# Kernel tuning notes

Measured on AMD Instinct MI355X. Metric: run time of the kernel, lower is better.

Reference implementation:

```python
import jax, jax.numpy as jnp
import numpy as np
import math

D_MODEL = 1024
NUM_HEADS = 16
HEAD_DIM = D_MODEL // NUM_HEADS
WINDOW = 5  # positions j with i - W//2 <= j <= i + W//2 are visible


def setup_inputs() -> dict:
    key = jax.random.key(0)
    ks = jax.random.split(key, 9)
    B, S = 2, 2048
    x = jax.random.normal(ks[0], (B, S, D_MODEL), dtype=jnp.float32)
    # Xavier-uniform linear weights [out, in] (torch convention), zero biases
    lim = math.sqrt(6.0 / (D_MODEL + D_MODEL))
    def w(k):
        return jax.random.uniform(k, (D_MODEL, D_MODEL), dtype=jnp.float32, minval=-lim, maxval=lim)
    return {
        'x': x,
        'Wq': w(ks[1]), 'bq': jnp.zeros((D_MODEL,), jnp.float32),
        'Wk': w(ks[2]), 'bk': jnp.zeros((D_MODEL,), jnp.float32),
        'Wv': w(ks[3]), 'bv': jnp.zeros((D_MODEL,), jnp.float32),
        'Wo': w(ks[4]), 'bo': jnp.zeros((D_MODEL,), jnp.float32),
    }


def reference(x, Wq, bq, Wk, bk, Wv, bv, Wo, bo):
    B, S, D = x.shape
    H, hd = NUM_HEADS, HEAD_DIM
    half = WINDOW // 2

    def proj(W, b):
        # torch Linear: y = x @ W.T + b ; split heads -> [B, H, S, hd]
        return (jnp.einsum('bsd,ed->bse', x, W) + b).reshape(B, S, H, hd).transpose(0, 2, 1, 3)

    q = proj(Wq, bq)
    k = proj(Wk, bk)
    v = proj(Wv, bv)

    scores = jnp.einsum('bhqd,bhkd->bhqk', q, k) / jnp.sqrt(jnp.asarray(hd, x.dtype))
    i = jnp.arange(S)[:, None]
    j = jnp.arange(S)[None, :]
    band = (j >= i - half) & (j <= i + half)  # [S, S] local window mask
    scores = jnp.where(band, scores, jnp.asarray(-1e9, x.dtype))
    attn = jax.nn.softmax(scores, axis=-1)  # dropout is identity in eval mode
    out = jnp.einsum('bhqk,bhkd->bhqd', attn, v)
    out = out.transpose(0, 2, 1, 3).reshape(B, S, D)
    return jnp.einsum('bsd,ed->bse', out, Wo) + bo
```

## Files before the change

### kernel.cpp

```cpp
#include <hip/hip_runtime.h>
#include <hip/hip_bf16.h>

typedef __bf16 bf16_t;
typedef __bf16 bf16x4 __attribute__((ext_vector_type(4)));
typedef __bf16 bf16x8 __attribute__((ext_vector_type(8)));
typedef float f32x4 __attribute__((ext_vector_type(4)));

#define S_LEN 2048
#define DMODEL 1024
#define NHEADS 16
#define HDIM 64
#define BROWS 4096
#define QKVN 3072

__device__ __forceinline__ void async16(const void* g, void* l) {
  __builtin_amdgcn_global_load_lds(
      (const __attribute__((address_space(1))) void*)g,
      (__attribute__((address_space(3))) void*)l, 16, 0, 0);
}

__global__ __launch_bounds__(256) void cvt_all_kernel(
    const float* __restrict__ x, const float* __restrict__ Wq,
    const float* __restrict__ Wk, const float* __restrict__ Wv,
    const float* __restrict__ Wo, bf16_t* __restrict__ dst) {
  const int i = blockIdx.x * 256 + threadIdx.x;
  constexpr int XN4 = (BROWS * DMODEL) / 4;
  constexpr int WN4 = (DMODEL * DMODEL) / 4;
  const float* src;
  size_t off;
  if (i < XN4) {
    src = x;
    off = (size_t)i;
  } else {
    const int wi = i - XN4;
    const int w = wi >> 18;
    off = (size_t)(wi & (WN4 - 1));
    src = (w == 0) ? Wq : (w == 1) ? Wk : (w == 2) ? Wv : Wo;
  }
  const float4 v = *(const float4*)(src + off * 4);
  bf16x4 o;
  o[0] = (bf16_t)v.x;
  o[1] = (bf16_t)v.y;
  o[2] = (bf16_t)v.z;
  o[3] = (bf16_t)v.w;
  *(bf16x4*)(dst + (size_t)i * 4) = o;
}

#define BARR __builtin_amdgcn_s_barrier()
#define SB0 __builtin_amdgcn_sched_barrier(0)
#define VMC3 asm volatile("s_waitcnt vmcnt(3)" ::: "memory")
#define VMC0 asm volatile("s_waitcnt vmcnt(0)" ::: "memory")

__global__ __launch_bounds__(512, 2) void gemm_qkv256_kernel(
    const bf16_t* __restrict__ A, const bf16_t* __restrict__ W,
    const float* __restrict__ bq, const float* __restrict__ bk,
    const float* __restrict__ bv, bf16_t* __restrict__ C) {
  constexpr int Kd = 1024;
  __shared__ char lds[114688];
  char* ldsA = lds;
  char* ldsB = lds + 65536;

  const int m0 = blockIdx.x * 256;
  const int n0 = blockIdx.y * 192;

  const int tid = threadIdx.x;
  const int lane = tid & 63;
  const int wid = tid >> 6;
  const int wr = wid >> 2;
  const int wc = wid & 3;
  const int fr = lane & 15;
  const int l16 = lane >> 4;

  f32x4 acc[8][3] = {};
  bf16x8 aS0[4][2], aS1[4][2], bB[3][2];

  auto stageA = [&](int buf, int h, int kt) {
#pragma unroll
    for (int l = 0; l < 2; ++l) {
      const int idx = l * 512 + tid;
      const int r = idx >> 3;
      const int slot = idx & 7;
      async16((const char*)(A + (size_t)(m0 + h * 128 + r) * Kd + kt * 64 +
                            ((slot ^ (r & 7)) << 3)),
              ldsA + buf * 32768 + h * 16384 + r * 128 + slot * 16);
    }
  };
  auto stageB = [&](int buf, int th, int kt) {
    const int r = tid >> 3;
    const int slot = tid & 7;
    async16((const char*)(W + (size_t)(n0 + th * 64 + r) * Kd + kt * 64 +
                          ((slot ^ (r & 7)) << 3)),
            ldsB + buf * 24576 + th * 8192 + r * 128 + slot * 16);
  };

  auto rdA = [&](int buf, int row, int ks) -> bf16x8 {
    return *(const bf16x8*)(ldsA + buf * 32768 + row * 128 +
                            ((((ks << 2) + l16) ^ (row & 7)) << 4));
  };
  auto rdB = [&](int buf, int row, int ks) -> bf16x8 {
    return *(const bf16x8*)(ldsB + buf * 24576 + row * 128 +
                            ((((ks << 2) + l16) ^ (row & 7)) << 4));
  };

#define RDA_TO(AS, MH, BUF)                                              \
  _Pragma("unroll") for (int m_ = 0; m_ < 4; ++m_)                       \
      _Pragma("unroll") for (int ks_ = 0; ks_ < 2; ++ks_) AS[m_][ks_] =  \
          rdA(BUF, wr * 128 + (MH)*64 + m_ * 16 + fr, ks_);
#define RDB(NF0, NC, BUF)                                                \
  _Pragma("unroll") for (int n_ = 0; n_ < (NC); ++n_)                    \
      _Pragma("unroll") for (int ks_ = 0; ks_ < 2; ++ks_)                \
          bB[(NF0) + n_][ks_] =                                          \
              rdB(BUF, wc * 48 + ((NF0) + n_) * 16 + fr, ks_);
#define MMAQ(AS, MH, NF0, NC)                                                 \
  _Pragma("unroll") for (int m_ = 0; m_ < 4; ++m_)                            \
      _Pragma("unroll") for (int n_ = 0; n_ < (NC); ++n_) {                   \
    acc[(MH)*4 + m_][(NF0) + n_] = __builtin_amdgcn_mfma_f32_16x16x32_bf16(   \
        AS[m_][0], bB[(NF0) + n_][0], acc[(MH)*4 + m_][(NF0) + n_], 0, 0, 0); \
    acc[(MH)*4 + m_][(NF0) + n_] = __builtin_amdgcn_mfma_f32_16x16x32_bf16(   \
        AS[m_][1], bB[(NF0) + n_][1], acc[(MH)*4 + m_][(NF0) + n_], 0, 0, 0); \
  }

  stageA(0, 0, 0);
  stageA(0, 1, 0);
  stageB(0, 0, 0);
  stageB(0, 1, 0);
  stageB(0, 2, 0);
  stageB(1, 0, 1);
  stageB(1, 1, 1);
  stageB(1, 2, 1);
  VMC3;
  BARR;

#pragma unroll 1
  for (int i = 0; i < 8; ++i) {
    const int t0 = 2 * i, t1 = 2 * i + 1;
    const bool st = (i < 7);
    RDA_TO(aS0, 0, 0);
    RDB(0, 2, 0);
    RDA_TO(aS1, 1, 0);
    stageA(1, 0, t1);
    SB0;
    BARR;
    __builtin_amdgcn_s_setprio(1);
    MMAQ(aS0, 0, 0, 2);
    __builtin_amdgcn_s_setprio(0);
    BARR;
    RDB(2, 1, 0);
    stageA(1, 1, t1);
    SB0;
    BARR;
    __builtin_amdgcn_s_setprio(1);
    MMAQ(aS0, 0, 2, 1);
    __builtin_amdgcn_s_setprio(0);
    BARR;
    if (st) stageB(0, 0, t0 + 2);
    SB0;
    BARR;
    __builtin_amdgcn_s_setprio(1);
    MMAQ(aS1, 1, 0, 2);
    __builtin_amdgcn_s_setprio(0);
    BARR;
    if (st) {
      stageB(0, 1, t0 + 2);
      stageB(0, 2, t0 + 2);
    }
    SB0;
    __builtin_amdgcn_s_setprio(1);
    MMAQ(aS1, 1, 2, 1);
    __builtin_amdgcn_s_setprio(0);
    SB0;
    if (st) {
      VMC3;
    } else {
      VMC0;
    }
    BARR;
    RDA_TO(aS0, 0, 1);
    RDB(0, 2, 1);
    RDA_TO(aS1, 1, 1);
    if (st) stageA(0, 0, t0 + 2);
    SB0;
    BARR;
    __builtin_amdgcn_s_setprio(1);
    MMAQ(aS0, 0, 0, 2);
    __builtin_amdgcn_s_setprio(0);
    BARR;
    RDB(2, 1, 1);
    if (st) stageA(0, 1, t0 + 2);
    SB0;
    BARR;
    __builtin_amdgcn_s_setprio(1);
    MMAQ(aS0, 0, 2, 1);
    __builtin_amdgcn_s_setprio(0);
    BARR;
    if (st) stageB(1, 0, t1 + 2);
    SB0;
    BARR;
    __builtin_amdgcn_s_setprio(1);
    MMAQ(aS1, 1, 0, 2);
    __builtin_amdgcn_s_setprio(0);
    BARR;
    if (st) {
      stageB(1, 1, t1 + 2);
      stageB(1, 2, t1 + 2);
    }
    SB0;
    __builtin_amdgcn_s_setprio(1);
    MMAQ(aS1, 1, 2, 1);
    __builtin_amdgcn_s_setprio(0);
    SB0;
    if (st) VMC3;
    BARR;
  }
#undef RDA_TO
#undef RDB
#undef MMAQ

  const int cr = l16 * 4;
#pragma unroll
  for (int nf = 0; nf < 3; ++nf) {
    const int col = n0 + wc * 48 + nf * 16 + fr;
    const int mat = col >> 10;
    const float* bp = (mat == 0) ? bq : (mat == 1) ? bk : bv;
    const float bval = bp[col & 1023];
#pragma unroll
    for (int mf = 0; mf < 8; ++mf) {
      const int row = m0 + wr * 128 + mf * 16 + cr;
#pragma unroll
      for (int r = 0; r < 4; ++r)
        C[(size_t)(row + r) * QKVN + col] = (bf16_t)(acc[mf][nf][r] + bval);
    }
  }
}

__global__ __launch_bounds__(512) void gemm_o_kernel(
    const bf16_t* __restrict__ Adat, const bf16_t* __restrict__ W,
    const float* __restrict__ bias, float* __restrict__ out) {
  constexpr int Kd = 1024, Nd = 1024, BK = 32, NT = Kd / BK;
  __shared__ bf16_t ldsA[2][128 * BK];
  __shared__ bf16_t ldsB[2][128 * BK];

  const int m0 = blockIdx.x * 128;
  const int n0 = blockIdx.y * 128;

  const int tid = threadIdx.x;
  const int lane = tid & 63;
  const int wid = tid >> 6;
  const int wr = wid >> 2;
  const int wc = wid & 3;
  const int fr = lane & 15;
  const int ko = (lane >> 4) * 8;

  f32x4 acc[4][2] = {};

  auto stage = [&](int buf, int t) {
    const int k0 = t * BK;
    const int row = tid >> 2;
    const int kb = (tid & 3) * 16;
    async16((const char*)(Adat + (size_t)(m0 + row) * Kd + k0) + kb,
            (char*)ldsA[buf] + row * 64 + kb);
    async16((const char*)(W + (size_t)(n0 + row) * Kd + k0) + kb,
            (char*)ldsB[buf] + row * 64 + kb);
  };

  auto compute = [&](int buf) {
    bf16x8 af[4], bf[2];
#pragma unroll
    for (int i = 0; i < 4; ++i)
      af[i] = *(const bf16x8*)(ldsA[buf] + (wr * 64 + i * 16 + fr) * BK + ko);
#pragma unroll
    for (int j = 0; j < 2; ++j)
      bf[j] = *(const bf16x8*)(ldsB[buf] + (wc * 32 + j * 16 + fr) * BK + ko);
#pragma unroll
    for (int i = 0; i < 4; ++i)
#pragma unroll
      for (int j = 0; j < 2; ++j)
        acc[i][j] = __builtin_amdgcn_mfma_f32_16x16x32_bf16(af[i], bf[j],
                                                            acc[i][j], 0, 0, 0);
  };

  stage(0, 0);
  __syncthreads();
#pragma unroll 1
  for (int t = 0; t < NT; ++t) {
    if (t + 1 < NT) stage((t + 1) & 1, t + 1);
    compute(t & 1);
    __syncthreads();
  }

  const int cr = (lane >> 4) * 4;
#pragma unroll
  for (int j = 0; j < 2; ++j) {
    const int col = n0 + wc * 32 + j * 16 + fr;
    const float bval = bias[col];
#pragma unroll
    for (int i = 0; i < 4; ++i) {
#pragma unroll
      for (int r = 0; r < 4; ++r) {
        const int row = m0 + wr * 64 + i * 16 + cr + r;
        out[(size_t)row * Nd + col] = acc[i][j][r] + bval;
      }
    }
  }
}

#define CHUNK 256
#define TROWS 260

__global__ __launch_bounds__(256) void attn_kernel(
    const bf16_t* __restrict__ QKV, bf16_t* __restrict__ ctx) {
  __shared__ bf16_t ldsK[TROWS * HDIM];
  __shared__ bf16_t ldsV[TROWS * HDIM];

  const int tid = threadIdx.x;
  const int blk = blockIdx.x;
  const int chunk = blk & 7;
  const int bh = blk >> 3;
  const int h = bh & (NHEADS - 1);
  const int b = bh >> 4;
  const int s0 = chunk * CHUNK;

  const bf16_t* Kb = QKV + (size_t)b * S_LEN * QKVN + DMODEL + h * HDIM;
  const bf16_t* Vb = QKV + (size_t)b * S_LEN * QKVN + 2 * DMODEL + h * HDIM;

#pragma unroll
  for (int j = 0; j < 9; ++j) {
    const int i = j * 256 + tid;
    if (i < TROWS * 8) {
      const int tr = i >> 3;
      const int slot = i & 7;
      const int c = slot ^ (tr & 7);
      int gs = s0 - 2 + tr;
      gs = (gs < 0) ? 0 : (gs >= S_LEN ? S_LEN - 1 : gs);
      async16((const char*)(Kb + (size_t)gs * QKVN) + c * 16,
              (char*)ldsK + i * 16);
      async16((const char*)(Vb + (size_t)gs * QKVN) + c * 16,
              (char*)ldsV + i * 16);
    }
  }

  const int s = s0 + tid;
  const bf16_t* Qrow = QKV + ((size_t)(b * S_LEN) + s) * QKVN + h * HDIM;
  bf16x8 q8[8];
#pragma unroll
  for (int c = 0; c < 8; ++c) q8[c] = *(const bf16x8*)(Qrow + c * 8);
  float qf[64];
#pragma unroll
  for (int c = 0; c < 8; ++c)
#pragma unroll
    for (int e = 0; e < 8; ++e) qf[c * 8 + e] = (float)q8[c][e];

  __syncthreads();

  float sc[5];
#pragma unroll
  for (int jj = 0; jj < 5; ++jj) {
    const int tr = tid + jj;
    float d = 0.f;
#pragma unroll
    for (int c = 0; c < 8; ++c) {
      const bf16x8 k8 = *(const bf16x8*)(ldsK + tr * HDIM + (c ^ (tr & 7)) * 8);
#pragma unroll
      for (int e = 0; e < 8; ++e) d += qf[c * 8 + e] * (float)k8[e];
    }
    const int j = s - 2 + jj;
    sc[jj] = (j < 0 || j >= S_LEN) ? -1e30f : d * 0.125f;
  }

  float m = sc[0];
#pragma unroll
  for (int jj = 1; jj < 5; ++jj) m = fmaxf(m, sc[jj]);
  float p[5], l = 0.f;
#pragma unroll
  for (int jj = 0; jj < 5; ++jj) {
    p[jj] = __expf(sc[jj] - m);
    l += p[jj];
  }
  const float inv = 1.0f / l;
#pragma unroll
  for (int jj = 0; jj < 5; ++jj) p[jj] *= inv;

  float o[64];
#pragma unroll
  for (int e = 0; e < 64; ++e) o[e] = 0.f;
#pragma unroll
  for (int jj = 0; jj < 5; ++jj) {
    const int tr = tid + jj;
    const float pj = p[jj];
#pragma unroll
    for (int c = 0; c < 8; ++c) {
      const bf16x8 v8 = *(const bf16x8*)(ldsV + tr * HDIM + (c ^ (tr & 7)) * 8);
#pragma unroll
      for (int e = 0; e < 8; ++e) o[c * 8 + e] += pj * (float)v8[e];
    }
  }

  bf16_t* Crow = (bf16_t*)ctx + ((size_t)(b * S_LEN) + s) * DMODEL + h * HDIM;
#pragma unroll
  for (int c = 0; c < 8; ++c) {
    bf16x8 ov;
#pragma unroll
    for (int e = 0; e < 8; ++e) ov[e] = (bf16_t)o[c * 8 + e];
    *(bf16x8*)(Crow + c * 8) = ov;
  }
}

extern "C" void kernel_launch(void* const* d_in, const int* in_sizes, int n_in,
                              void* d_out, int out_size, void* d_ws,
                              size_t ws_size, hipStream_t stream) {
  const float* x = (const float*)d_in[0];
  const float* Wq = (const float*)d_in[1];
  const float* bq = (const float*)d_in[2];
  const float* Wk = (const float*)d_in[3];
  const float* bk = (const float*)d_in[4];
  const float* Wv = (const float*)d_in[5];
  const float* bv = (const float*)d_in[6];
  const float* Wo = (const float*)d_in[7];
  const float* bo = (const float*)d_in[8];
  float* out = (float*)d_out;

  const size_t mat = (size_t)BROWS * DMODEL;
  const size_t wmat = (size_t)DMODEL * DMODEL;
  bf16_t* xb = (bf16_t*)d_ws;
  bf16_t* Wqkv = xb + mat;
  bf16_t* Wob = Wqkv + 3 * wmat;
  bf16_t* QKV = Wob + wmat;
  bf16_t* ctx = QKV + 3 * mat;

  cvt_all_kernel<<<8192, 256, 0, stream>>>(x, Wq, Wk, Wv, Wo, xb);
  gemm_qkv256_kernel<<<dim3(16, 16), 512, 0, stream>>>(xb, Wqkv, bq, bk, bv,
                                                       QKV);
  attn_kernel<<<256, 256, 0, stream>>>(QKV, ctx);
  gemm_o_kernel<<<dim3(32, 8), 512, 0, stream>>>(ctx, Wob, bo, out);
}
```

Before: 78.20 us.

## Simplify QKV GEMM main loop to whole-tile double-buffered pipeline

Replaces the hand-interleaved 8-phase loop, which split LDS reads, async global-to-LDS staging and MFMA groups across many barriers and sched_barriers, with a simple per-k-tile loop. Each iteration reads all A and B fragments from LDS, waits on lgkmcnt, issues the next-next tile's async loads into the same buffer, then runs all MFMAs and waits on vmcnt(7) before a barrier. This cuts the barrier count and scheduling constraints. In exchange it loses the fine-grained overlap of LDS reads with MFMA, and it holds more fragment registers live at once.

```diff
diff --git a/kernel.cpp b/kernel.cpp
--- a/kernel.cpp
+++ b/kernel.cpp
@@ -47,8 +47,8 @@
 }
 
 #define BARR __builtin_amdgcn_s_barrier()
-#define SB0 __builtin_amdgcn_sched_barrier(0)
-#define VMC3 asm volatile("s_waitcnt vmcnt(3)" ::: "memory")
+#define LGKM0 asm volatile("s_waitcnt lgkmcnt(0)" ::: "memory")
+#define VMC7 asm volatile("s_waitcnt vmcnt(7)" ::: "memory")
 #define VMC0 asm volatile("s_waitcnt vmcnt(0)" ::: "memory")
 
 __global__ __launch_bounds__(512, 2) void gemm_qkv256_kernel(
@@ -102,119 +102,67 @@
                             ((((ks << 2) + l16) ^ (row & 7)) << 4));
   };
 
-#define RDA_TO(AS, MH, BUF)                                              \
-  _Pragma("unroll") for (int m_ = 0; m_ < 4; ++m_)                       \
-      _Pragma("unroll") for (int ks_ = 0; ks_ < 2; ++ks_) AS[m_][ks_] =  \
-          rdA(BUF, wr * 128 + (MH)*64 + m_ * 16 + fr, ks_);
-#define RDB(NF0, NC, BUF)                                                \
-  _Pragma("unroll") for (int n_ = 0; n_ < (NC); ++n_)                    \
-      _Pragma("unroll") for (int ks_ = 0; ks_ < 2; ++ks_)                \
-          bB[(NF0) + n_][ks_] =                                          \
-              rdB(BUF, wc * 48 + ((NF0) + n_) * 16 + fr, ks_);
-#define MMAQ(AS, MH, NF0, NC)                                                 \
-  _Pragma("unroll") for (int m_ = 0; m_ < 4; ++m_)                            \
-      _Pragma("unroll") for (int n_ = 0; n_ < (NC); ++n_) {                   \
-    acc[(MH)*4 + m_][(NF0) + n_] = __builtin_amdgcn_mfma_f32_16x16x32_bf16(   \
-        AS[m_][0], bB[(NF0) + n_][0], acc[(MH)*4 + m_][(NF0) + n_], 0, 0, 0); \
-    acc[(MH)*4 + m_][(NF0) + n_] = __builtin_amdgcn_mfma_f32_16x16x32_bf16(   \
-        AS[m_][1], bB[(NF0) + n_][1], acc[(MH)*4 + m_][(NF0) + n_], 0, 0, 0); \
-  }
-
   stageA(0, 0, 0);
   stageA(0, 1, 0);
   stageB(0, 0, 0);
   stageB(0, 1, 0);
   stageB(0, 2, 0);
+  stageA(1, 0, 1);
+  stageA(1, 1, 1);
   stageB(1, 0, 1);
   stageB(1, 1, 1);
   stageB(1, 2, 1);
-  VMC3;
+  VMC7;
   BARR;
 
 #pragma unroll 1
-  for (int i = 0; i < 8; ++i) {
-    const int t0 = 2 * i, t1 = 2 * i + 1;
-    const bool st = (i < 7);
-    RDA_TO(aS0, 0, 0);
-    RDB(0, 2, 0);
-    RDA_TO(aS1, 1, 0);
-    stageA(1, 0, t1);
-    SB0;
+  for (int t = 0; t < 16; ++t) {
+    const int buf = t & 1;
+#pragma unroll
+    for (int m_ = 0; m_ < 4; ++m_)
+#pragma unroll
+      for (int ks_ = 0; ks_ < 2; ++ks_) {
+        aS0[m_][ks_] = rdA(buf, wr * 128 + m_ * 16 + fr, ks_);
+        aS1[m_][ks_] = rdA(buf, wr * 128 + 64 + m_ * 16 + fr, ks_);
+      }
+#pragma unroll
+    for (int n_ = 0; n_ < 3; ++n_)
+#pragma unroll
+      for (int ks_ = 0; ks_ < 2; ++ks_)
+        bB[n_][ks_] = rdB(buf, wc * 48 + n_ * 16 + fr, ks_);
+    LGKM0;
     BARR;
+    if (t + 2 < 16) {
+      stageA(buf, 0, t + 2);
+      stageA(buf, 1, t + 2);
+      stageB(buf, 0, t + 2);
+      stageB(buf, 1, t + 2);
+      stageB(buf, 2, t + 2);
+    }
     __builtin_amdgcn_s_setprio(1);
-    MMAQ(aS0, 0, 0, 2);
+#pragma unroll
+    for (int m_ = 0; m_ < 4; ++m_)
+#pragma unroll
+      for (int n_ = 0; n_ < 3; ++n_) {
+#pragma unroll
+        for (int ks_ = 0; ks_ < 2; ++ks_)
+          acc[m_][n_] = __builtin_amdgcn_mfma_f32_16x16x32_bf16(
+              aS0[m_][ks_], bB[n_][ks_], acc[m_][n_], 0, 0, 0);
+#pragma unroll
+        for (int ks_ = 0; ks_ < 2; ++ks_)
+          acc[4 + m_][n_] = __builtin_amdgcn_mfma_f32_16x16x32_bf16(
+              aS1[m_][ks_], bB[n_][ks_], acc[4 + m_][n_], 0, 0, 0);
+      }
     __builtin_amdgcn_s_setprio(0);
-    BARR;
-    RDB(2, 1, 0);
-    stageA(1, 1, t1);
-    SB0;
-    BARR;
-    __builtin_amdgcn_s_setprio(1);
-    MMAQ(aS0, 0, 2, 1);
-    __builtin_amdgcn_s_setprio(0);
-    BARR;
-    if (st) stageB(0, 0, t0 + 2);
-    SB0;
-    BARR;
-    __builtin_amdgcn_s_setprio(1);
-    MMAQ(aS1, 1, 0, 2);
-    __builtin_amdgcn_s_setprio(0);
-    BARR;
-    if (st) {
-      stageB(0, 1, t0 + 2);
-      stageB(0, 2, t0 + 2);
-    }
-    SB0;
-    __builtin_amdgcn_s_setprio(1);
-    MMAQ(aS1, 1, 2, 1);
-    __builtin_amdgcn_s_setprio(0);
-    SB0;
-    if (st) {
-      VMC3;
-    } else {
-      VMC0;
-    }
-    BARR;
-    RDA_TO(aS0, 0, 1);
-    RDB(0, 2, 1);
-    RDA_TO(aS1, 1, 1);
-    if (st) stageA(0, 0, t0 + 2);
-    SB0;
-    BARR;
-    __builtin_amdgcn_s_setprio(1);
-    MMAQ(aS0, 0, 0, 2);
-    __builtin_amdgcn_s_setprio(0);
-    BARR;
-    RDB(2, 1, 1);
-    if (st) stageA(0, 1, t0 + 2);
-    SB0;
-    BARR;
-    __builtin_amdgcn_s_setprio(1);
-    MMAQ(aS0, 0, 2, 1);
-    __builtin_amdgcn_s_setprio(0);
-    BARR;
-    if (st) stageB(1, 0, t1 + 2);
-    SB0;
-    BARR;
-    __builtin_amdgcn_s_setprio(1);
-    MMAQ(aS1, 1, 0, 2);
-    __builtin_amdgcn_s_setprio(0);
-    BARR;
-    if (st) {
-      stageB(1, 1, t1 + 2);
-      stageB(1, 2, t1 + 2);
-    }
-    SB0;
-    __builtin_amdgcn_s_setprio(1);
-    MMAQ(aS1, 1, 2, 1);
-    __builtin_amdgcn_s_setprio(0);
-    SB0;
-    if (st) VMC3;
-    BARR;
-  }
-#undef RDA_TO
-#undef RDB
-#undef MMAQ
+    if (t < 15) {
+      if (t + 2 < 16) {
+        VMC7;
+      } else {
+        VMC0;
+      }
+      BARR;
+    }
+  }
 
   const int cr = l16 * 4;
 #pragma unroll
```

After: 77.41 us. About the same (-1.0%).
